# Optimization experiments

Hardware: AMD Instinct MI355X
Metric: run time of the kernel (lower is better)

The kernel has to match this reference:

```python
import jax, jax.numpy as jnp
import numpy as np

B, S, HID, NH = 4, 2048, 1024, 16
DH = HID // NH  # 64
SCALE = 1.0 / float(np.sqrt(DH))


def _linear_params(key, scale=0.02):
    kw, kb = jax.random.split(key)
    W = jax.random.normal(kw, (HID, HID), dtype=jnp.float32) * scale
    b = jax.random.normal(kb, (HID,), dtype=jnp.float32) * scale
    return W, b


def setup_inputs() -> dict:
    key = jax.random.key(0)
    ks = jax.random.split(key, 9)
    x = jax.random.normal(ks[0], (B, S, HID), dtype=jnp.float32)
    reasoning_mask = jax.random.uniform(ks[1], (B, S, 1, 1), dtype=jnp.float32)
    Wq, bq = _linear_params(ks[2])
    Wk, bk = _linear_params(ks[3])
    Wv, bv = _linear_params(ks[4])
    Wqr, bqr = _linear_params(ks[5])
    Wkr, bkr = _linear_params(ks[6])
    Wo, bo = _linear_params(ks[7])
    return {"x": x, "reasoning_mask": reasoning_mask,
            "Wq": Wq, "bq": bq, "Wk": Wk, "bk": bk, "Wv": Wv, "bv": bv,
            "Wqr": Wqr, "bqr": bqr, "Wkr": Wkr, "bkr": bkr, "Wo": Wo, "bo": bo}


def reference(x, reasoning_mask, Wq, bq, Wk, bk, Wv, bv, Wqr, bqr, Wkr, bkr, Wo, bo):
    # Projections: x @ W + b, then view (B, S, NH, DH)
    def proj(W, b):
        return (jnp.einsum('bsh,hd->bsd', x, W) + b).reshape(B, S, NH, DH)

    q = proj(Wq, bq)
    k = proj(Wk, bk)
    v = proj(Wv, bv)
    q_r = proj(Wqr, bqr)
    k_r = proj(Wkr, bkr)

    # Reasoning-gated blend of standard and reasoning projections
    q = q * (1.0 - reasoning_mask) + q_r * reasoning_mask
    k = k * (1.0 - reasoning_mask) + k_r * reasoning_mask

    # Faithful to source: matmul over the LAST two dims of (B,S,NH,DH),
    # i.e. per-token attention ACROSS HEADS -> scores shape (B,S,NH,NH)
    scores = jnp.einsum('bshd,bsed->bshe', q, k) * SCALE
    attn = jax.nn.softmax(scores, axis=-1)  # dropout is identity at eval
    out = jnp.einsum('bshe,bsed->bshd', attn, v)  # (B,S,NH,DH)

    # Faithful transpose(1,2) + contiguous view to (B, S, HID)
    out = jnp.transpose(out, (0, 2, 1, 3)).reshape(B, -1, HID)
    return jnp.einsum('bsh,hd->bsd', out, Wo) + bo
```

## Files before the change

kernel.cpp:

```cpp
#include <hip/hip_runtime.h>
#include <hip/hip_bf16.h>


typedef __attribute__((ext_vector_type(8))) short short8;
typedef __attribute__((ext_vector_type(4))) short short4v;
typedef __attribute__((ext_vector_type(4))) float f32x4;

#define HID 1024
#define NTOK 8192
#define WT_ELEMS (1024 * 1024)

__device__ __forceinline__ short f2bs(float f) {
  __hip_bfloat16 h = __float2bfloat16(f);
  return *reinterpret_cast<short*>(&h);
}
__device__ __forceinline__ float bs2f(short s) {
  __hip_bfloat16 h;
  *reinterpret_cast<short*>(&h) = s;
  return __bfloat162float(h);
}
__device__ __forceinline__ void gload16(const void* g, void* l) {
  __builtin_amdgcn_global_load_lds(
      (const __attribute__((address_space(1))) void*)g,
      (__attribute__((address_space(3))) void*)l, 16, 0, 0);
}

#define BAR() asm volatile("s_barrier" ::: "memory")
#define VMWAIT(N) asm volatile("s_waitcnt vmcnt(" #N ")" ::: "memory")
#define PRIO1 __builtin_amdgcn_s_setprio(1)
#define PRIO0 __builtin_amdgcn_s_setprio(0)

__global__ __launch_bounds__(256) void prep_kernel(
    const float* __restrict__ W0, const float* __restrict__ W1,
    const float* __restrict__ W2, const float* __restrict__ W3,
    const float* __restrict__ W4, const float* __restrict__ W5,
    const float* __restrict__ X, short* __restrict__ WT, short* __restrict__ XB)
{
  __shared__ short sT[64][68];
  const int bid = blockIdx.x, tid = threadIdx.x;
  if (bid < 1536) {
    const int z = bid >> 8, rem = bid & 255;
    const float* W = z == 0 ? W0 : z == 1 ? W1 : z == 2 ? W2 : z == 3 ? W3
                   : z == 4 ? W4 : W5;
    short* OUT = WT + (size_t)z * WT_ELEMS;
    const int k0 = (rem & 15) * 64, n0 = (rem >> 4) * 64;
    #pragma unroll
    for (int i = 0; i < 4; i++) {
      const int li = tid + i * 256;
      const int kr = li >> 4, c4 = (li & 15) << 2;
      const f32x4 wv = *reinterpret_cast<const f32x4*>(&W[(size_t)(k0 + kr) * HID + n0 + c4]);
      short4v s4;
      #pragma unroll
      for (int j = 0; j < 4; j++) s4[j] = f2bs(wv[j]);
      *reinterpret_cast<short4v*>(&sT[kr][c4]) = s4;
    }
    __syncthreads();
    #pragma unroll
    for (int i = 0; i < 4; i++) {
      const int li = tid + i * 256;
      const int nr = li >> 4, k4 = (li & 15) << 2;
      short4v o;
      #pragma unroll
      for (int j = 0; j < 4; j++) o[j] = sT[k4 + j][nr];
      const int kcol = (k0 + k4) ^ ((nr & 7) << 3);
      *reinterpret_cast<short4v*>(&OUT[(size_t)(n0 + nr) * HID + kcol]) = o;
    }
  } else {
    const int gid = (bid - 1536) * 256 + tid;
    const int row = gid >> 7, kc = (gid & 127) << 3;
    const f32x4 a = *reinterpret_cast<const f32x4*>(&X[(size_t)row * HID + kc]);
    const f32x4 b = *reinterpret_cast<const f32x4*>(&X[(size_t)row * HID + kc + 4]);
    short8 s;
    #pragma unroll
    for (int j = 0; j < 4; j++) { s[j] = f2bs(a[j]); s[4 + j] = f2bs(b[j]); }
    const int phys = (kc & ~63) | ((kc & 63) ^ ((row & 7) << 3));
    *reinterpret_cast<short8*>(&XB[(size_t)row * HID + phys]) = s;
  }
}

__global__ __launch_bounds__(512, 2) void gated8_kernel(
    const short* __restrict__ XB, const short* __restrict__ WTbase,
    const float* __restrict__ bq, const float* __restrict__ bqr,
    const float* __restrict__ bk, const float* __restrict__ bkr,
    const float* __restrict__ MASK,
    __hip_bfloat16* __restrict__ qg, __hip_bfloat16* __restrict__ kg)
{
  __shared__ short lA[2][256][64];
  __shared__ short lB1[2][128][64];
  __shared__ short lB2[2][128][64];

  const int z = blockIdx.z;
  const short* W1T = WTbase + (size_t)(2 * z) * WT_ELEMS;
  const short* W2T = W1T + WT_ELEMS;
  const float* B1b = z ? bk : bq;
  const float* B2b = z ? bkr : bqr;
  __hip_bfloat16* OUT = z ? kg : qg;

  const int m0 = blockIdx.x * 256, n0 = blockIdx.y * 128;
  const int tid = threadIdx.x, lane = tid & 63, w = tid >> 6;
  const int wr = (w >> 1) * 64, wc = (w & 1) * 64;
  const int lrow = lane & 15, lkhi = (lane >> 4) << 3;
  const int swz = (lrow & 7) << 3;
  const int srow = lane >> 3, scol = (lane & 7) << 3;

  f32x4 acc1[4][4] = {}, acc2[4][4] = {};
  short8 bf1k[2][4], bf2k[2][4];
  short8 af00, af01, af10, af11;

  auto stA2 = [&](int slot, int kt, int i0) {
    const int k0 = kt * 64;
    #pragma unroll
    for (int i = 0; i < 2; i++) {
      const int chunk = w * 4 + i0 + i;
      gload16(&XB[(size_t)(m0 + chunk * 8 + srow) * HID + k0 + scol],
              &lA[slot][chunk * 8][0]);
    }
  };
  auto stB1s = [&](int slot, int kt) {
    const int k0 = kt * 64;
    #pragma unroll
    for (int i = 0; i < 2; i++) {
      const int chunk = w * 2 + i;
      gload16(&W1T[(size_t)(n0 + chunk * 8 + srow) * HID + k0 + scol],
              &lB1[slot][chunk * 8][0]);
    }
  };
  auto stB2s = [&](int slot, int kt) {
    const int k0 = kt * 64;
    #pragma unroll
    for (int i = 0; i < 2; i++) {
      const int chunk = w * 2 + i;
      gload16(&W2T[(size_t)(n0 + chunk * 8 + srow) * HID + k0 + scol],
              &lB2[slot][chunk * 8][0]);
    }
  };
  auto rdA = [&](int s, int m, int kk) -> short8 {
    const int lk = (kk * 32 + lkhi) ^ swz;
    return *reinterpret_cast<const short8*>(&lA[s][wr + m * 16 + lrow][lk]);
  };

#define RDBF(S, KK)                                                                   \
  _Pragma("unroll")                                                                   \
  for (int n = 0; n < 4; n++) {                                                       \
    const int lk = ((KK) * 32 + lkhi) ^ swz;                                          \
    bf1k[KK][n] = *reinterpret_cast<const short8*>(&lB1[S][wc + n * 16 + lrow][lk]);  \
    bf2k[KK][n] = *reinterpret_cast<const short8*>(&lB2[S][wc + n * 16 + lrow][lk]);  \
  }
#define MM16(MB, A0, A1, KB)                                                                           \
  _Pragma("unroll")                                                                                    \
  for (int n = 0; n < 4; n++) {                                                                        \
    acc1[MB][n]     = __builtin_amdgcn_mfma_f32_16x16x32_bf16(A0, bf1k[KB][n], acc1[MB][n], 0, 0, 0);     \
    acc1[MB + 1][n] = __builtin_amdgcn_mfma_f32_16x16x32_bf16(A1, bf1k[KB][n], acc1[MB + 1][n], 0, 0, 0); \
    acc2[MB][n]     = __builtin_amdgcn_mfma_f32_16x16x32_bf16(A0, bf2k[KB][n], acc2[MB][n], 0, 0, 0);     \
    acc2[MB + 1][n] = __builtin_amdgcn_mfma_f32_16x16x32_bf16(A1, bf2k[KB][n], acc2[MB + 1][n], 0, 0, 0); \
  }
#define GHALF(S, SN, TS)                                    \
  stA2(SN, TS, 0);                                          \
  VMWAIT(2);                                                \
  BAR();                                                    \
  af00 = rdA(S, 0, 0); af01 = rdA(S, 1, 0);                 \
  RDBF(S, 0);                                               \
  af10 = rdA(S, 2, 0); af11 = rdA(S, 3, 0);                 \
  stA2(SN, TS, 2);                                          \
  BAR();                                                    \
  PRIO1; MM16(0, af00, af01, 0); PRIO0;                     \
  BAR();                                                    \
  af00 = rdA(S, 0, 1); af01 = rdA(S, 1, 1);                 \
  RDBF(S, 1);                                               \
  stB1s(SN, TS);                                            \
  BAR();                                                    \
  PRIO1; MM16(2, af10, af11, 0); PRIO0;                     \
  BAR();                                                    \
  af10 = rdA(S, 2, 1); af11 = rdA(S, 3, 1);                 \
  stB2s(SN, TS);                                            \
  BAR();                                                    \
  PRIO1; MM16(0, af00, af01, 1); PRIO0;                     \
  BAR();                                                    \
  PRIO1; MM16(2, af10, af11, 1); PRIO0;                     \
  BAR();

  stA2(0, 0, 0); stA2(0, 0, 2); stB1s(0, 0); stB2s(0, 0);

  #pragma unroll 1
  for (int i = 0; i < 8; i++) {
    const int tb = 2 * i + 1;
    const int tn = (i < 7) ? 2 * i + 2 : 15;
    GHALF(0, 1, tb)
    GHALF(1, 0, tn)
  }
  VMWAIT(0);
#undef GHALF
#undef MM16
#undef RDBF

  #pragma unroll
  for (int m = 0; m < 4; m++) {
    const int rbase = m0 + wr + m * 16 + ((lane >> 4) << 2);
    #pragma unroll
    for (int n = 0; n < 4; n++) {
      const int col = n0 + wc + n * 16 + lrow;
      const float bias1 = B1b[col];
      const float bias2 = B2b[col];
      #pragma unroll
      for (int r = 0; r < 4; r++) {
        const int row = rbase + r;
        const float mk = MASK[row];
        const float val = (acc1[m][n][r] + bias1) * (1.f - mk) +
                          (acc2[m][n][r] + bias2) * mk;
        OUT[(size_t)row * HID + col] = __float2bfloat16(val);
      }
    }
  }
}

template<bool OUTF32>
__global__ __launch_bounds__(512, 2) void plain8_kernel(
    const short* __restrict__ A, const short* __restrict__ WT,
    const float* __restrict__ BIAS, void* __restrict__ OUTv)
{
  __shared__ short lA[2][256][64];
  __shared__ short lB[2][128][64];

  const int m0 = blockIdx.x * 256, n0 = blockIdx.y * 128;
  const int tid = threadIdx.x, lane = tid & 63, w = tid >> 6;
  const int wr = (w >> 1) * 64, wc = (w & 1) * 64;
  const int lrow = lane & 15, lkhi = (lane >> 4) << 3;
  const int swz = (lrow & 7) << 3;
  const int srow = lane >> 3, scol = (lane & 7) << 3;

  f32x4 acc[4][4] = {};
  short8 paf[2][4], pbf[2][4];

  auto stTrip = [&](int slot, int kt, int t) {
    const int k0 = kt * 64;
    if (t == 0) {
      #pragma unroll
      for (int i = 0; i < 3; i++) {
        const int chunk = w * 4 + i;
        gload16(&A[(size_t)(m0 + chunk * 8 + srow) * HID + k0 + scol],
                &lA[slot][chunk * 8][0]);
      }
    } else {
      const int chunk = w * 4 + 3;
      gload16(&A[(size_t)(m0 + chunk * 8 + srow) * HID + k0 + scol],
              &lA[slot][chunk * 8][0]);
      #pragma unroll
      for (int i = 0; i < 2; i++) {
        const int bchunk = w * 2 + i;
        gload16(&WT[(size_t)(n0 + bchunk * 8 + srow) * HID + k0 + scol],
                &lB[slot][bchunk * 8][0]);
      }
    }
  };

#define RDP(S, KK)                                                                    \
  _Pragma("unroll")                                                                   \
  for (int m = 0; m < 4; m++) {                                                       \
    const int lk = ((KK) * 32 + lkhi) ^ swz;                                          \
    paf[KK][m] = *reinterpret_cast<const short8*>(&lA[S][wr + m * 16 + lrow][lk]);    \
    pbf[KK][m] = *reinterpret_cast<const short8*>(&lB[S][wc + m * 16 + lrow][lk]);    \
  }
#define PMM16(KK)                                                                     \
  _Pragma("unroll")                                                                   \
  for (int m = 0; m < 4; m++)                                                         \
    _Pragma("unroll")                                                                 \
    for (int n = 0; n < 4; n++)                                                       \
      acc[m][n] = __builtin_amdgcn_mfma_f32_16x16x32_bf16(paf[KK][m], pbf[KK][n], acc[m][n], 0, 0, 0);
#define PHALF(S, SN, TS)        \
  stTrip(SN, TS, 0);            \
  VMWAIT(3);                    \
  BAR();                        \
  RDP(S, 0)                     \
  RDP(S, 1)                     \
  stTrip(SN, TS, 1);            \
  BAR();                        \
  PRIO1; PMM16(0) PRIO0;        \
  BAR();                        \
  PRIO1; PMM16(1) PRIO0;        \
  BAR();

  stTrip(0, 0, 0); stTrip(0, 0, 1);

  #pragma unroll 1
  for (int i = 0; i < 8; i++) {
    const int tb = 2 * i + 1;
    const int tn = (i < 7) ? 2 * i + 2 : 15;
    PHALF(0, 1, tb)
    PHALF(1, 0, tn)
  }
  VMWAIT(0);
#undef PHALF
#undef PMM16
#undef RDP

  #pragma unroll
  for (int m = 0; m < 4; m++) {
    const int rbase = m0 + wr + m * 16 + ((lane >> 4) << 2);
    #pragma unroll
    for (int n = 0; n < 4; n++) {
      const int col = n0 + wc + n * 16 + lrow;
      const float bias = BIAS[col];
      #pragma unroll
      for (int r = 0; r < 4; r++) {
        const float val = acc[m][n][r] + bias;
        const size_t oidx = (size_t)(rbase + r) * HID + col;
        if (OUTF32) ((float*)OUTv)[oidx] = val;
        else ((__hip_bfloat16*)OUTv)[oidx] = __float2bfloat16(val);
      }
    }
  }
}

__global__ __launch_bounds__(256) void attn_kernel(
    const __hip_bfloat16* __restrict__ Q, const __hip_bfloat16* __restrict__ K,
    const __hip_bfloat16* __restrict__ V, __hip_bfloat16* __restrict__ O)
{
  const int t = blockIdx.x;
  const int b = t >> 11, s = t & 2047;
  __shared__ float sQ[16][68], sK[16][68], sV[16][68];
  __shared__ float sA[16][17];
  const int tid = threadIdx.x;
  const size_t tb = (size_t)t * HID;

  {
    const int h = tid >> 4, d0 = (tid & 15) << 2;
    const int o = (h << 6) + d0;
    const short4v qv = *reinterpret_cast<const short4v*>(&((const short*)Q)[tb + o]);
    const short4v kv = *reinterpret_cast<const short4v*>(&((const short*)K)[tb + o]);
    const short4v vv = *reinterpret_cast<const short4v*>(&((const short*)V)[tb + o]);
    #pragma unroll
    for (int j = 0; j < 4; j++) {
      sQ[h][d0 + j] = bs2f(qv[j]);
      sK[h][d0 + j] = bs2f(kv[j]);
      sV[h][d0 + j] = bs2f(vv[j]);
    }
  }
  __syncthreads();

  const int h = tid >> 4, e = tid & 15;
  float sc = 0.f;
  #pragma unroll
  for (int d = 0; d < 64; d++) sc += sQ[h][d] * sK[e][d];
  sc *= 0.125f;

  float mx = sc;
  mx = fmaxf(mx, __shfl_xor(mx, 1));
  mx = fmaxf(mx, __shfl_xor(mx, 2));
  mx = fmaxf(mx, __shfl_xor(mx, 4));
  mx = fmaxf(mx, __shfl_xor(mx, 8));
  const float p = __expf(sc - mx);
  float sm = p;
  sm += __shfl_xor(sm, 1);
  sm += __shfl_xor(sm, 2);
  sm += __shfl_xor(sm, 4);
  sm += __shfl_xor(sm, 8);
  sA[h][e] = p / sm;
  __syncthreads();

  const int row7 = (s >> 4) & 7;
  const size_t ob = ((size_t)b * 2048 + (s >> 4)) * HID + ((size_t)(s & 15) << 6);
  {
    const int hh = tid >> 4, d4 = (tid & 15) << 2;
    f32x4 o = {0.f, 0.f, 0.f, 0.f};
    #pragma unroll
    for (int e2 = 0; e2 < 16; e2++) {
      const float a = sA[hh][e2];
      #pragma unroll
      for (int j = 0; j < 4; j++) o[j] += a * sV[e2][d4 + j];
    }
    short4v ov;
    #pragma unroll
    for (int j = 0; j < 4; j++) ov[j] = f2bs(o[j]);
    *reinterpret_cast<short4v*>(
        &((short*)O)[ob + (size_t)hh * 128 * HID + (d4 ^ (row7 << 3))]) = ov;
  }
}

extern "C" void kernel_launch(void* const* d_in, const int* in_sizes, int n_in,
                              void* d_out, int out_size, void* d_ws, size_t ws_size,
                              hipStream_t stream) {
  (void)in_sizes; (void)n_in; (void)out_size; (void)ws_size;
  const float* x   = (const float*)d_in[0];
  const float* rm  = (const float*)d_in[1];
  const float* Wq  = (const float*)d_in[2];
  const float* bq  = (const float*)d_in[3];
  const float* Wk  = (const float*)d_in[4];
  const float* bk  = (const float*)d_in[5];
  const float* Wv  = (const float*)d_in[6];
  const float* bv  = (const float*)d_in[7];
  const float* Wqr = (const float*)d_in[8];
  const float* bqr = (const float*)d_in[9];
  const float* Wkr = (const float*)d_in[10];
  const float* bkr = (const float*)d_in[11];
  const float* Wo  = (const float*)d_in[12];
  const float* bo  = (const float*)d_in[13];

  char* ws = (char*)d_ws;
  short* wt = (short*)ws;
  __hip_bfloat16* qg = (__hip_bfloat16*)(ws + 12u * 1024 * 1024);
  __hip_bfloat16* vv = (__hip_bfloat16*)(ws + 28u * 1024 * 1024);
  __hip_bfloat16* ar = (__hip_bfloat16*)(ws + 44u * 1024 * 1024);
  short* xb = (short*)d_out;
  __hip_bfloat16* kg = (__hip_bfloat16*)((char*)d_out + 16u * 1024 * 1024);

  prep_kernel<<<dim3(5632), 256, 0, stream>>>(Wq, Wqr, Wk, Wkr, Wv, Wo, x, wt, xb);
  gated8_kernel<<<dim3(32, 8, 2), 512, 0, stream>>>(xb, wt, bq, bqr, bk, bkr, rm, qg, kg);
  plain8_kernel<false><<<dim3(32, 8), 512, 0, stream>>>(xb, wt + (size_t)4 * WT_ELEMS, bv, vv);
  attn_kernel<<<dim3(NTOK), 256, 0, stream>>>(qg, kg, vv, ar);
  plain8_kernel<true><<<dim3(32, 8), 512, 0, stream>>>((const short*)ar,
                                                       wt + (size_t)5 * WT_ELEMS, bo, d_out);
}
```

Baseline: 165.7 us.

## Restructure GEMM main loops into per-k-half phases with explicit lgkm waits

Reworks the software pipeline of both the gated dual-weight GEMM and the plain GEMM. Each K tile now runs as phases that read A and B fragments, issue the next tile's global-to-LDS loads, wait on lgkmcnt(0) with scheduling barriers, then run MFMAs. The full vmcnt(0) wait moves to the end of each tile instead of partial waits at the start. This cuts register use for the fragment arrays and makes the instruction schedule predictable, at the cost of less overlap between LDS reads and MFMAs and a stricter wait on outstanding global loads.

```diff
diff --git a/kernel.cpp b/kernel.cpp
--- a/kernel.cpp
+++ b/kernel.cpp
@@ -27,8 +27,12 @@
 
 #define BAR() asm volatile("s_barrier" ::: "memory")
 #define VMWAIT(N) asm volatile("s_waitcnt vmcnt(" #N ")" ::: "memory")
+#define LGKM0 do { asm volatile("s_waitcnt lgkmcnt(0)" ::: "memory"); \
+                   __builtin_amdgcn_sched_barrier(0); } while (0)
+#define SCB __builtin_amdgcn_sched_barrier(0)
 #define PRIO1 __builtin_amdgcn_s_setprio(1)
 #define PRIO0 __builtin_amdgcn_s_setprio(0)
+#define MFMA16x16 __builtin_amdgcn_mfma_f32_16x16x32_bf16
 
 __global__ __launch_bounds__(256) void prep_kernel(
     const float* __restrict__ W0, const float* __restrict__ W1,
@@ -104,8 +108,8 @@
   const int srow = lane >> 3, scol = (lane & 7) << 3;
 
   f32x4 acc1[4][4] = {}, acc2[4][4] = {};
-  short8 bf1k[2][4], bf2k[2][4];
-  short8 af00, af01, af10, af11;
+  short8 bf1k[4], bf2k[4];
+  short8 af0, af1, af2, af3;
 
   auto stA2 = [&](int slot, int kt, int i0) {
     const int k0 = kt * 64;
@@ -139,59 +143,79 @@
     return *reinterpret_cast<const short8*>(&lA[s][wr + m * 16 + lrow][lk]);
   };
 
-#define RDBF(S, KK)                                                                   \
+#define RDB1(S, KK)                                                                   \
   _Pragma("unroll")                                                                   \
   for (int n = 0; n < 4; n++) {                                                       \
     const int lk = ((KK) * 32 + lkhi) ^ swz;                                          \
-    bf1k[KK][n] = *reinterpret_cast<const short8*>(&lB1[S][wc + n * 16 + lrow][lk]);  \
-    bf2k[KK][n] = *reinterpret_cast<const short8*>(&lB2[S][wc + n * 16 + lrow][lk]);  \
-  }
-#define MM16(MB, A0, A1, KB)                                                                           \
-  _Pragma("unroll")                                                                                    \
-  for (int n = 0; n < 4; n++) {                                                                        \
-    acc1[MB][n]     = __builtin_amdgcn_mfma_f32_16x16x32_bf16(A0, bf1k[KB][n], acc1[MB][n], 0, 0, 0);     \
-    acc1[MB + 1][n] = __builtin_amdgcn_mfma_f32_16x16x32_bf16(A1, bf1k[KB][n], acc1[MB + 1][n], 0, 0, 0); \
-    acc2[MB][n]     = __builtin_amdgcn_mfma_f32_16x16x32_bf16(A0, bf2k[KB][n], acc2[MB][n], 0, 0, 0);     \
-    acc2[MB + 1][n] = __builtin_amdgcn_mfma_f32_16x16x32_bf16(A1, bf2k[KB][n], acc2[MB + 1][n], 0, 0, 0); \
-  }
-#define GHALF(S, SN, TS)                                    \
-  stA2(SN, TS, 0);                                          \
-  VMWAIT(2);                                                \
-  BAR();                                                    \
-  af00 = rdA(S, 0, 0); af01 = rdA(S, 1, 0);                 \
-  RDBF(S, 0);                                               \
-  af10 = rdA(S, 2, 0); af11 = rdA(S, 3, 0);                 \
-  stA2(SN, TS, 2);                                          \
-  BAR();                                                    \
-  PRIO1; MM16(0, af00, af01, 0); PRIO0;                     \
-  BAR();                                                    \
-  af00 = rdA(S, 0, 1); af01 = rdA(S, 1, 1);                 \
-  RDBF(S, 1);                                               \
-  stB1s(SN, TS);                                            \
-  BAR();                                                    \
-  PRIO1; MM16(2, af10, af11, 0); PRIO0;                     \
-  BAR();                                                    \
-  af10 = rdA(S, 2, 1); af11 = rdA(S, 3, 1);                 \
-  stB2s(SN, TS);                                            \
-  BAR();                                                    \
-  PRIO1; MM16(0, af00, af01, 1); PRIO0;                     \
-  BAR();                                                    \
-  PRIO1; MM16(2, af10, af11, 1); PRIO0;                     \
+    bf1k[n] = *reinterpret_cast<const short8*>(&lB1[S][wc + n * 16 + lrow][lk]);      \
+  }
+#define RDB2(S, KK)                                                                   \
+  _Pragma("unroll")                                                                   \
+  for (int n = 0; n < 4; n++) {                                                       \
+    const int lk = ((KK) * 32 + lkhi) ^ swz;                                          \
+    bf2k[n] = *reinterpret_cast<const short8*>(&lB2[S][wc + n * 16 + lrow][lk]);      \
+  }
+#define MM16A                                                             \
+  _Pragma("unroll")                                                       \
+  for (int n = 0; n < 4; n++) {                                           \
+    acc1[0][n] = MFMA16x16(af0, bf1k[n], acc1[0][n], 0, 0, 0);            \
+    acc1[1][n] = MFMA16x16(af1, bf1k[n], acc1[1][n], 0, 0, 0);            \
+    acc1[2][n] = MFMA16x16(af2, bf1k[n], acc1[2][n], 0, 0, 0);            \
+    acc1[3][n] = MFMA16x16(af3, bf1k[n], acc1[3][n], 0, 0, 0);            \
+  }
+#define MM16B                                                             \
+  _Pragma("unroll")                                                       \
+  for (int n = 0; n < 4; n++) {                                           \
+    acc2[0][n] = MFMA16x16(af0, bf2k[n], acc2[0][n], 0, 0, 0);            \
+    acc2[1][n] = MFMA16x16(af1, bf2k[n], acc2[1][n], 0, 0, 0);            \
+    acc2[2][n] = MFMA16x16(af2, bf2k[n], acc2[2][n], 0, 0, 0);            \
+    acc2[3][n] = MFMA16x16(af3, bf2k[n], acc2[3][n], 0, 0, 0);            \
+  }
+#define GTILE(S, SN, TS)                                                 \
+                         \
+  af0 = rdA(S, 0, 0); af1 = rdA(S, 1, 0);                                \
+  af2 = rdA(S, 2, 0); af3 = rdA(S, 3, 0);                                \
+  RDB1(S, 0);                                                            \
+  stA2(SN, TS, 0); stA2(SN, TS, 2);                                      \
+  BAR(); LGKM0;                                                          \
+  PRIO1; MM16A PRIO0; SCB;                                               \
+  BAR();                                                                 \
+                         \
+  RDB2(S, 0);                                                            \
+  stB1s(SN, TS); stB2s(SN, TS);                                          \
+  BAR(); LGKM0;                                                          \
+  PRIO1; MM16B PRIO0; SCB;                                               \
+  BAR();                                                                 \
+                                          \
+  af0 = rdA(S, 0, 1); af1 = rdA(S, 1, 1);                                \
+  af2 = rdA(S, 2, 1); af3 = rdA(S, 3, 1);                                \
+  RDB1(S, 1);                                                            \
+  BAR(); LGKM0;                                                          \
+  PRIO1; MM16A PRIO0; SCB;                                               \
+  BAR();                                                                 \
+                       \
+  RDB2(S, 1);                                                            \
+  BAR(); LGKM0;                                                          \
+  PRIO1; MM16B PRIO0; SCB;                                               \
+  VMWAIT(0);                                                             \
   BAR();
 
   stA2(0, 0, 0); stA2(0, 0, 2); stB1s(0, 0); stB2s(0, 0);
+  VMWAIT(0);
+  BAR();
 
   #pragma unroll 1
   for (int i = 0; i < 8; i++) {
     const int tb = 2 * i + 1;
     const int tn = (i < 7) ? 2 * i + 2 : 15;
-    GHALF(0, 1, tb)
-    GHALF(1, 0, tn)
-  }
-  VMWAIT(0);
-#undef GHALF
-#undef MM16
-#undef RDBF
+    GTILE(0, 1, tb)
+    GTILE(1, 0, tn)
+  }
+#undef GTILE
+#undef MM16A
+#undef MM16B
+#undef RDB1
+#undef RDB2
 
   #pragma unroll
   for (int m = 0; m < 4; m++) {
@@ -229,7 +253,7 @@
   const int srow = lane >> 3, scol = (lane & 7) << 3;
 
   f32x4 acc[4][4] = {};
-  short8 paf[2][4], pbf[2][4];
+  short8 paf[4], pbf[4];
 
   auto stTrip = [&](int slot, int kt, int t) {
     const int k0 = kt * 64;
@@ -257,39 +281,42 @@
   _Pragma("unroll")                                                                   \
   for (int m = 0; m < 4; m++) {                                                       \
     const int lk = ((KK) * 32 + lkhi) ^ swz;                                          \
-    paf[KK][m] = *reinterpret_cast<const short8*>(&lA[S][wr + m * 16 + lrow][lk]);    \
-    pbf[KK][m] = *reinterpret_cast<const short8*>(&lB[S][wc + m * 16 + lrow][lk]);    \
-  }
-#define PMM16(KK)                                                                     \
+    paf[m] = *reinterpret_cast<const short8*>(&lA[S][wr + m * 16 + lrow][lk]);        \
+    pbf[m] = *reinterpret_cast<const short8*>(&lB[S][wc + m * 16 + lrow][lk]);        \
+  }
+#define PMM16                                                                         \
   _Pragma("unroll")                                                                   \
   for (int m = 0; m < 4; m++)                                                         \
     _Pragma("unroll")                                                                 \
     for (int n = 0; n < 4; n++)                                                       \
-      acc[m][n] = __builtin_amdgcn_mfma_f32_16x16x32_bf16(paf[KK][m], pbf[KK][n], acc[m][n], 0, 0, 0);
-#define PHALF(S, SN, TS)        \
+      acc[m][n] = MFMA16x16(paf[m], pbf[n], acc[m][n], 0, 0, 0);
+#define PTILE(S, SN, TS)        \
+                        \
+  RDP(S, 0)                     \
   stTrip(SN, TS, 0);            \
-  VMWAIT(3);                    \
+  BAR(); LGKM0;                 \
+  PRIO1; PMM16 PRIO0; SCB;      \
   BAR();                        \
-  RDP(S, 0)                     \
+                        \
   RDP(S, 1)                     \
   stTrip(SN, TS, 1);            \
-  BAR();                        \
-  PRIO1; PMM16(0) PRIO0;        \
-  BAR();                        \
-  PRIO1; PMM16(1) PRIO0;        \
+  BAR(); LGKM0;                 \
+  PRIO1; PMM16 PRIO0; SCB;      \
+  VMWAIT(0);                    \
   BAR();
 
   stTrip(0, 0, 0); stTrip(0, 0, 1);
+  VMWAIT(0);
+  BAR();
 
   #pragma unroll 1
   for (int i = 0; i < 8; i++) {
     const int tb = 2 * i + 1;
     const int tn = (i < 7) ? 2 * i + 2 : 15;
-    PHALF(0, 1, tb)
-    PHALF(1, 0, tn)
-  }
-  VMWAIT(0);
-#undef PHALF
+    PTILE(0, 1, tb)
+    PTILE(1, 0, tn)
+  }
+#undef PTILE
 #undef PMM16
 #undef RDP
 
```

Result: faster. 152.3 us (-8.1%).
